# Kernel optimization log

Hardware: AMD Instinct MI355X
Metric: run time of the kernel (lower is better)

## Reference

```python
import jax, jax.numpy as jnp
import numpy as np

PC_RANGE = (0.0, -40.0, -3.0, 70.4, 40.0, 1.0)
N, C, M, L = 200000, 64, 50000, 2000000
H = W = 176  # bev grid bound for synthetic pillar indices


def setup_inputs() -> dict:
    key = jax.random.key(0)
    k1, k2, k3, k4, k5, k6 = jax.random.split(key, 6)
    # points live in relative coords in [0, range_extent)
    ext = jnp.array([PC_RANGE[3] - PC_RANGE[0], PC_RANGE[4] - PC_RANGE[1], PC_RANGE[5] - PC_RANGE[2]], jnp.float32)
    xyz = jax.random.uniform(k1, (N, 3), jnp.float32) * ext
    point_features = jax.random.normal(k2, (N, C), jnp.float32)
    pillar_centers = jax.random.uniform(k3, (M, 3), jnp.float32) * ext
    pillar_indices = jax.random.randint(k4, (M, 3), 0, H, jnp.int32)
    point_set_indices = jax.random.randint(k5, (L,), 0, N, jnp.int32)
    pillar_set_indices = jnp.sort(jax.random.randint(k6, (L,), 0, M, jnp.int32))
    return {
        "xyz": xyz,
        "point_features": point_features,
        "pillar_centers": pillar_centers,
        "pillar_indices": pillar_indices,
        "point_set_indices": point_set_indices,
        "pillar_set_indices": pillar_set_indices,
    }


def reference(xyz, point_features, pillar_centers, pillar_indices, point_set_indices, pillar_set_indices):
    # gather per-pair features / coords
    group_point_features = jnp.take(point_features, point_set_indices, axis=0)   # (L, C)
    group_point_xyz = jnp.take(xyz, point_set_indices, axis=0)                   # (L, 3)
    group_pillar_centers = jnp.take(pillar_centers, pillar_set_indices, axis=0)  # (L, 3)
    # offset of each point from its pillar center (relative coords)
    rel = group_point_xyz - group_pillar_centers                                 # (L, 3)
    # shift point coords to absolute frame
    offset = jnp.array([PC_RANGE[0], PC_RANGE[1], PC_RANGE[2]], group_point_xyz.dtype)
    absl = group_point_xyz + offset                                              # (L, 3)
    group_features = jnp.concatenate([group_point_features, absl, rel], axis=1)  # (L, C+6)
    indice2bev = jnp.ones((1,), jnp.float32)  # bev_flag=False path
    return pillar_indices, pillar_set_indices, group_features, indice2bev
```

## Files before the change

### kernel.cpp

```cpp
#include <hip/hip_runtime.h>

constexpr int       kM = 50000;
constexpr long long kL = 2000000;
constexpr int       kRowLen = 70;
constexpr int       kTileRows = 64;

constexpr long long kOutPillarIdx = 0;
constexpr long long kOutPsi       = 150000;
constexpr long long kOutGF        = 2150000;
constexpr long long kOutBev       = 142150000;

__global__ void int_to_float_kernel(const int* __restrict__ in,
                                    float* __restrict__ out, int n) {
    int i = blockIdx.x * blockDim.x + threadIdx.x;
    int stride = gridDim.x * blockDim.x;
    for (; i < n; i += stride) out[i] = (float)in[i];
}

__global__ void int4_to_float4_kernel(const int4* __restrict__ in,
                                      float4* __restrict__ out, int n4) {
    int i = blockIdx.x * blockDim.x + threadIdx.x;
    int stride = gridDim.x * blockDim.x;
    for (; i < n4; i += stride) {
        int4 v = in[i];
        out[i] = make_float4((float)v.x, (float)v.y, (float)v.z, (float)v.w);
    }
}

__global__ void bev_flag_kernel(float* __restrict__ out) {
    out[0] = 1.0f;
}

__global__ __launch_bounds__(256, 8)
void group_features_kernel(const float* __restrict__ xyz,
                           const float4* __restrict__ pf4,
                           const float* __restrict__ pc,
                           const int*  __restrict__ point_set_idx,
                           const int*  __restrict__ pillar_set_idx,
                           float* __restrict__ out) {
    __shared__ float s[kTileRows * kRowLen];

    const int tid  = threadIdx.x;
    const long long row0 = (long long)blockIdx.x * kTileRows;

    {
        const int j = tid & 15;
        const int rsub = tid >> 4;
        #pragma unroll
        for (int it = 0; it < 4; ++it) {
            const int r = it * 16 + rsub;
            const int p = point_set_idx[row0 + r];
            const float4 v = pf4[(long long)p * 16 + j];
            float* dst = &s[r * kRowLen + j * 4];
            dst[0] = v.x; dst[1] = v.y; dst[2] = v.z; dst[3] = v.w;
        }
    }

    if (tid < kTileRows * 3) {
        const int r = tid / 3;
        const int c = tid - r * 3;
        const int p = point_set_idx[row0 + r];
        const int q = pillar_set_idx[row0 + r];
        const float x  = xyz[(long long)p * 3 + c];
        const float pcv = pc[(long long)q * 3 + c];
        const float off = (c == 0) ? 0.0f : ((c == 1) ? -40.0f : -3.0f);
        s[r * kRowLen + 64 + c] = x + off;
        s[r * kRowLen + 67 + c] = x - pcv;
    }

    __syncthreads();

    {
        const float4* s4 = (const float4*)s;
        float4* o4 = (float4*)(out + row0 * kRowLen);
        constexpr int n4 = kTileRows * kRowLen / 4;
        #pragma unroll
        for (int it = 0; it < 5; ++it) {
            const int k = it * 256 + tid;
            if (k < n4) o4[k] = s4[k];
        }
    }
}

extern "C" void kernel_launch(void* const* d_in, const int* in_sizes, int n_in,
                              void* d_out, int out_size, void* d_ws, size_t ws_size,
                              hipStream_t stream) {
    const float* xyz             = (const float*)d_in[0];
    const float* point_features  = (const float*)d_in[1];
    const float* pillar_centers  = (const float*)d_in[2];
    const int*   pillar_indices  = (const int*)d_in[3];
    const int*   point_set_idx   = (const int*)d_in[4];
    const int*   pillar_set_idx  = (const int*)d_in[5];

    float* out = (float*)d_out;

    {
        int n4 = kM * 3 / 4;
        int blocks = (n4 + 255) / 256;
        int4_to_float4_kernel<<<blocks, 256, 0, stream>>>(
            (const int4*)pillar_indices, (float4*)(out + kOutPillarIdx), n4);
    }
    {
        int n4 = (int)(kL / 4);
        int blocks = 1024;
        int4_to_float4_kernel<<<blocks, 256, 0, stream>>>(
            (const int4*)pillar_set_idx, (float4*)(out + kOutPsi), n4);
    }
    {
        int blocks = (int)(kL / kTileRows);
        group_features_kernel<<<blocks, 256, 0, stream>>>(
            xyz, (const float4*)point_features, pillar_centers,
            point_set_idx, pillar_set_idx, out + kOutGF);
    }
    bev_flag_kernel<<<1, 1, 0, stream>>>(out + kOutBev);
}
```

Measured before the change: 199.6 us.

## Fuse index conversions and bev flag into group kernel; use per-wave tiles

Replaces the four launches (two int-to-float conversions, the grouping kernel and the bev flag write) with a single fused kernel. A few threads in each block handle the psi and pillar-index conversion slices and the bev flag. The tile is also split into per-wave 16-row slices written only by their own wave, which removes the __syncthreads barrier, and shared-memory writes now use float2 stores. This saves launch overhead and block-wide synchronisation. In exchange, correctness without a barrier depends on wave-synchronous execution, and a few lanes in every block do extra work.

```diff
diff --git a/kernel.cpp b/kernel.cpp
--- a/kernel.cpp
+++ b/kernel.cpp
@@ -3,80 +3,91 @@
 constexpr int       kM = 50000;
 constexpr long long kL = 2000000;
 constexpr int       kRowLen = 70;
-constexpr int       kTileRows = 64;
 
 constexpr long long kOutPillarIdx = 0;
 constexpr long long kOutPsi       = 150000;
 constexpr long long kOutGF        = 2150000;
 constexpr long long kOutBev       = 142150000;
 
-__global__ void int_to_float_kernel(const int* __restrict__ in,
-                                    float* __restrict__ out, int n) {
-    int i = blockIdx.x * blockDim.x + threadIdx.x;
-    int stride = gridDim.x * blockDim.x;
-    for (; i < n; i += stride) out[i] = (float)in[i];
-}
-
-__global__ void int4_to_float4_kernel(const int4* __restrict__ in,
-                                      float4* __restrict__ out, int n4) {
-    int i = blockIdx.x * blockDim.x + threadIdx.x;
-    int stride = gridDim.x * blockDim.x;
-    for (; i < n4; i += stride) {
-        int4 v = in[i];
-        out[i] = make_float4((float)v.x, (float)v.y, (float)v.z, (float)v.w);
-    }
-}
-
-__global__ void bev_flag_kernel(float* __restrict__ out) {
-    out[0] = 1.0f;
-}
+constexpr int kRowsPerWave = 16;
+constexpr int kWaves       = 4;
+constexpr int kTileRows    = kRowsPerWave * kWaves;
+constexpr int kGrid        = (int)(kL / kTileRows);
+constexpr int kPillarIdx4  = kM * 3 / 4;
 
 __global__ __launch_bounds__(256, 8)
-void group_features_kernel(const float* __restrict__ xyz,
-                           const float4* __restrict__ pf4,
-                           const float* __restrict__ pc,
-                           const int*  __restrict__ point_set_idx,
-                           const int*  __restrict__ pillar_set_idx,
-                           float* __restrict__ out) {
+void pillar_group_fused_kernel(const float* __restrict__ xyz,
+                               const float4* __restrict__ pf4,
+                               const float* __restrict__ pc,
+                               const int4*  __restrict__ pillar_idx4,
+                               const int4*  __restrict__ psi4,
+                               const int*   __restrict__ point_set_idx,
+                               const int*   __restrict__ pillar_set_idx,
+                               float* __restrict__ out) {
     __shared__ float s[kTileRows * kRowLen];
 
     const int tid  = threadIdx.x;
-    const long long row0 = (long long)blockIdx.x * kTileRows;
+    const int wave = tid >> 6;
+    const int lane = tid & 63;
+    const int row0 = blockIdx.x * kTileRows + wave * kRowsPerWave;
+    float* sw = &s[wave * kRowsPerWave * kRowLen];
+
+    if (tid < 16) {
+        int k = blockIdx.x * 16 + tid;
+        int4 v = psi4[k];
+        ((float4*)(out + kOutPsi))[k] =
+            make_float4((float)v.x, (float)v.y, (float)v.z, (float)v.w);
+    } else if (tid == 16) {
+        int k = blockIdx.x;
+        if (k < kPillarIdx4) {
+            int4 v = pillar_idx4[k];
+            ((float4*)(out + kOutPillarIdx))[k] =
+                make_float4((float)v.x, (float)v.y, (float)v.z, (float)v.w);
+        }
+    } else if (tid == 17) {
+        int k = kGrid + blockIdx.x;
+        if (k < kPillarIdx4) {
+            int4 v = pillar_idx4[k];
+            ((float4*)(out + kOutPillarIdx))[k] =
+                make_float4((float)v.x, (float)v.y, (float)v.z, (float)v.w);
+        }
+    } else if (tid == 18 && blockIdx.x == 0) {
+        out[kOutBev] = 1.0f;
+    }
 
     {
-        const int j = tid & 15;
-        const int rsub = tid >> 4;
+        const int j    = lane & 15;
+        const int rsub = lane >> 4;
         #pragma unroll
         for (int it = 0; it < 4; ++it) {
-            const int r = it * 16 + rsub;
+            const int r = it * 4 + rsub;
             const int p = point_set_idx[row0 + r];
             const float4 v = pf4[(long long)p * 16 + j];
-            float* dst = &s[r * kRowLen + j * 4];
-            dst[0] = v.x; dst[1] = v.y; dst[2] = v.z; dst[3] = v.w;
+            float* dst = &sw[r * kRowLen + j * 4];
+            *(float2*)(dst)     = make_float2(v.x, v.y);
+            *(float2*)(dst + 2) = make_float2(v.z, v.w);
         }
     }
 
-    if (tid < kTileRows * 3) {
-        const int r = tid / 3;
-        const int c = tid - r * 3;
+    if (lane < kRowsPerWave * 3) {
+        const int r = lane / 3;
+        const int c = lane - r * 3;
         const int p = point_set_idx[row0 + r];
         const int q = pillar_set_idx[row0 + r];
-        const float x  = xyz[(long long)p * 3 + c];
+        const float x   = xyz[(long long)p * 3 + c];
         const float pcv = pc[(long long)q * 3 + c];
         const float off = (c == 0) ? 0.0f : ((c == 1) ? -40.0f : -3.0f);
-        s[r * kRowLen + 64 + c] = x + off;
-        s[r * kRowLen + 67 + c] = x - pcv;
+        sw[r * kRowLen + 64 + c] = x + off;
+        sw[r * kRowLen + 67 + c] = x - pcv;
     }
 
-    __syncthreads();
-
     {
-        const float4* s4 = (const float4*)s;
-        float4* o4 = (float4*)(out + row0 * kRowLen);
-        constexpr int n4 = kTileRows * kRowLen / 4;
+        const float4* s4 = (const float4*)sw;
+        float4* o4 = (float4*)(out + kOutGF + (long long)row0 * kRowLen);
+        constexpr int n4 = kRowsPerWave * kRowLen / 4;
         #pragma unroll
         for (int it = 0; it < 5; ++it) {
-            const int k = it * 256 + tid;
+            const int k = it * 64 + lane;
             if (k < n4) o4[k] = s4[k];
         }
     }
@@ -94,23 +105,8 @@
 
     float* out = (float*)d_out;
 
-    {
-        int n4 = kM * 3 / 4;
-        int blocks = (n4 + 255) / 256;
-        int4_to_float4_kernel<<<blocks, 256, 0, stream>>>(
-            (const int4*)pillar_indices, (float4*)(out + kOutPillarIdx), n4);
-    }
-    {
-        int n4 = (int)(kL / 4);
-        int blocks = 1024;
-        int4_to_float4_kernel<<<blocks, 256, 0, stream>>>(
-            (const int4*)pillar_set_idx, (float4*)(out + kOutPsi), n4);
-    }
-    {
-        int blocks = (int)(kL / kTileRows);
-        group_features_kernel<<<blocks, 256, 0, stream>>>(
-            xyz, (const float4*)point_features, pillar_centers,
-            point_set_idx, pillar_set_idx, out + kOutGF);
-    }
-    bev_flag_kernel<<<1, 1, 0, stream>>>(out + kOutBev);
+    pillar_group_fused_kernel<<<kGrid, 256, 0, stream>>>(
+        xyz, (const float4*)point_features, pillar_centers,
+        (const int4*)pillar_indices, (const int4*)pillar_set_idx,
+        point_set_idx, pillar_set_idx, out);
 }
```

New measurement: 199.2 us. About the same (-0.2%).
